# Performance work log

Hardware: AMD Instinct MI355X
Metric: run time of the kernel (lower is better)

The kernel has to match this reference:

```python
import jax, jax.numpy as jnp
import numpy as np

T, B, F_, H, D, C = 16, 1024, 512, 128, 8, 100  # trees, batch, feat, hidden, depth, classes
L = 2 ** (D + 1)  # n_leaf = 512


def _routing_tables():
    # Static per-leaf routing: node index and branch side at each depth.
    # Derived from compute_mu's gather indices:
    #   node(d, l) = 2^d - 1 + l // 2^(D+1-d);  side(d, l) = (l // 2^(D-d)) % 2
    l = np.arange(L)
    node = np.stack([(2 ** d - 1) + l // (2 ** (D + 1 - d)) for d in range(D + 1)])  # [D+1, L]
    side = np.stack([(l // (2 ** (D - d))) % 2 for d in range(D + 1)])               # [D+1, L]
    return jnp.asarray(node, dtype=jnp.int32), jnp.asarray(side.astype(np.bool_))


def setup_inputs() -> dict:
    key = jax.random.key(0)
    ks = jax.random.split(key, 4)
    return {
        "feat": jax.random.normal(ks[0], (B, F_), jnp.float32),
        "W1": jax.random.normal(ks[1], (T, F_, H), jnp.float32) * 0.05,
        "b1": jnp.zeros((T, H), jnp.float32),
        "W2": jax.random.normal(ks[2], (T, H, L), jnp.float32) * 0.05,
        "b2": jnp.zeros((T, L), jnp.float32),
        "pi": jax.random.uniform(ks[3], (T, L, C), jnp.float32, -2.0, 2.0),
    }


def reference(feat, W1, b1, W2, b2, pi):
    node, side = _routing_tables()
    # Per-tree MLP head (dropout is identity in eval mode).
    h = jax.nn.relu(jnp.einsum('bf,tfh->tbh', feat, W1) + b1[:, None, :])        # [T,B,H]
    p = jax.nn.sigmoid(jnp.einsum('tbh,thl->tbl', h, W2) + b2[:, None, :])       # [T,B,L]
    # compute_mu: product of routing probs along each root->leaf path.
    sel = p[:, :, node]                          # [T,B,D+1,L] gather (static indices)
    route = jnp.where(side, 1.0 - sel, sel)      # left -> p, right -> 1-p
    mu = jnp.prod(route, axis=2)                 # [T,B,L]
    # compute_py_x: mean over leaves then mean over trees of mu @ softmax(pi).
    leaf_p = jax.nn.softmax(pi, axis=-1)         # [T,L,C]
    py_x = jnp.einsum('tbl,tlc->bc', mu, leaf_p) / (L * T)  # [B,C]
    return jnp.log(py_x)
```

## Files before the change

### kernel.cpp

```cpp
#include <hip/hip_runtime.h>
#include <hip/hip_bf16.h>
#include <math.h>

#define T_ 16
#define B_ 1024
#define F_ 512
#define H_ 128
#define D_ 8
#define C_ 100
#define L_ 512
#define CP_ 112

typedef __attribute__((ext_vector_type(8))) short bf16x8_t;
typedef __attribute__((ext_vector_type(4))) short bf16x4_t;
typedef __attribute__((ext_vector_type(4))) float f32x4_t;

__device__ inline ushort f2bf(float x) {
  __hip_bfloat16 b = __float2bfloat16(x);
  return *(ushort*)&b;
}
__device__ inline float bf2f(ushort u) {
  union { unsigned int i; float f; } v;
  v.i = ((unsigned int)u) << 16;
  return v.f;
}

__global__ __launch_bounds__(256) void k_prep(
    const float* __restrict__ feat, const float* __restrict__ W1,
    const float* __restrict__ W2, const float* __restrict__ pi,
    ushort* __restrict__ feat_bf, ushort* __restrict__ W1T,
    ushort* __restrict__ W2T, ushort* __restrict__ lp) {
  __shared__ float tile[32][33];
  const int bid = blockIdx.x, tid = threadIdx.x;

  if (bid < 256) {
    int i = (bid * 256 + tid) * 8;
    float4 a = *(const float4*)(feat + i);
    float4 b = *(const float4*)(feat + i + 4);
    bf16x8_t o;
    o[0] = (short)f2bf(a.x); o[1] = (short)f2bf(a.y);
    o[2] = (short)f2bf(a.z); o[3] = (short)f2bf(a.w);
    o[4] = (short)f2bf(b.x); o[5] = (short)f2bf(b.y);
    o[6] = (short)f2bf(b.z); o[7] = (short)f2bf(b.w);
    *(bf16x8_t*)(feat_bf + i) = o;
    return;
  }
  if (bid < 2304) {
    const float* X; ushort* XT; int K, N, kb, nb, s;
    if (bid < 1280) {
      int r = bid - 256;  kb = r & 15; nb = (r >> 4) & 3;  s = r >> 6;
      X = W1; XT = W1T; K = F_; N = H_;
    } else {
      int r = bid - 1280; kb = r & 3;  nb = (r >> 2) & 15; s = r >> 6;
      X = W2; XT = W2T; K = H_; N = L_;
    }
    const int k0 = kb * 32, n0 = nb * 32;
    const int c = tid & 31, r0 = tid >> 5;
    const float* Xs = X + (size_t)s * K * N;
    ushort* XTs = XT + (size_t)s * N * K;
#pragma unroll
    for (int j = 0; j < 4; ++j)
      tile[r0 + 8 * j][c] = Xs[(size_t)(k0 + r0 + 8 * j) * N + n0 + c];
    __syncthreads();
#pragma unroll
    for (int j = 0; j < 4; ++j)
      XTs[(size_t)(n0 + r0 + 8 * j) * K + k0 + c] = f2bf(tile[c][r0 + 8 * j]);
    return;
  }
  {
    int row  = (bid - 2304) * 4 + (tid >> 6);
    int lane = tid & 63;
    const float* x = pi + (size_t)row * C_;
    float v0 = (lane < C_) ? x[lane] : -1e30f;
    float v1 = (lane + 64 < C_) ? x[lane + 64] : -1e30f;
    float m = fmaxf(v0, v1);
#pragma unroll
    for (int off = 32; off; off >>= 1) m = fmaxf(m, __shfl_xor(m, off, 64));
    float e0 = __expf(v0 - m);
    float e1 = (lane + 64 < C_) ? __expf(v1 - m) : 0.0f;
    float sm = e0 + e1;
#pragma unroll
    for (int off = 32; off; off >>= 1) sm += __shfl_xor(sm, off, 64);
    float inv = 1.0f / sm;
    size_t base = (size_t)row * CP_;
    if (lane < C_) lp[base + lane] = f2bf(e0 * inv);
    int c2 = lane + 64;
    if (c2 < CP_) lp[base + c2] = f2bf(c2 < C_ ? e1 * inv : 0.0f);
  }
}

__global__ __launch_bounds__(256) void k12_mfma(
    const ushort* __restrict__ feat, const ushort* __restrict__ W1T,
    const float* __restrict__ b1, const ushort* __restrict__ W2T,
    const float* __restrict__ b2, ushort* __restrict__ mu) {
  __shared__ ushort smem[29696];
  ushort (*h_s)[136] = (ushort(*)[136])smem;
  ushort (*a_s)[72]  = (ushort(*)[72])(smem + 4352);
  ushort (*b_s)[72]  = (ushort(*)[72])(smem + 6656);
  ushort (*w_s)[136] = (ushort(*)[136])(smem + 4352);
  ushort (*p_s)[520] = (ushort(*)[520])(smem + 13056);

  const int t = blockIdx.y, b0 = blockIdx.x * 32, tid = threadIdx.x;
  const int w = tid >> 6, lane = tid & 63, quad = lane >> 4, n = lane & 15;

  {
    f32x4_t acc[2][2];
#pragma unroll
    for (int i = 0; i < 2; ++i)
#pragma unroll
      for (int j = 0; j < 2; ++j) acc[i][j] = (f32x4_t){0.f, 0.f, 0.f, 0.f};

    for (int kc = 0; kc < 8; ++kc) {
      __syncthreads();
      {
        int row = tid >> 3, col8 = (tid & 7) * 8;
        *(bf16x8_t*)&a_s[row][col8] =
            *(const bf16x8_t*)(feat + (size_t)(b0 + row) * F_ + kc * 64 + col8);
      }
#pragma unroll
      for (int i = 0; i < 4; ++i) {
        int idx = i * 256 + tid;
        int row = idx >> 3, col8 = (idx & 7) * 8;
        *(bf16x8_t*)&b_s[row][col8] =
            *(const bf16x8_t*)(W1T + ((size_t)t * H_ + row) * F_ + kc * 64 + col8);
      }
      __syncthreads();
#pragma unroll
      for (int ks = 0; ks < 64; ks += 32) {
        bf16x8_t af[2], bfr[2];
#pragma unroll
        for (int mt = 0; mt < 2; ++mt)
          af[mt] = *(const bf16x8_t*)&a_s[mt * 16 + n][ks + quad * 8];
#pragma unroll
        for (int nt = 0; nt < 2; ++nt)
          bfr[nt] = *(const bf16x8_t*)&b_s[w * 32 + nt * 16 + n][ks + quad * 8];
#pragma unroll
        for (int mt = 0; mt < 2; ++mt)
#pragma unroll
          for (int nt = 0; nt < 2; ++nt)
            acc[mt][nt] = __builtin_amdgcn_mfma_f32_16x16x32_bf16(
                af[mt], bfr[nt], acc[mt][nt], 0, 0, 0);
      }
    }
    float bias[2] = {b1[t * H_ + w * 32 + n], b1[t * H_ + w * 32 + 16 + n]};
#pragma unroll
    for (int mt = 0; mt < 2; ++mt)
#pragma unroll
      for (int nt = 0; nt < 2; ++nt)
#pragma unroll
        for (int r = 0; r < 4; ++r) {
          int row = mt * 16 + quad * 4 + r;
          int col = w * 32 + nt * 16 + n;
          float v = acc[mt][nt][r] + bias[nt];
          h_s[row][col] = f2bf(v > 0.f ? v : 0.f);
        }
  }

  for (int nc = 0; nc < 8; ++nc) {
    __syncthreads();
#pragma unroll
    for (int i = 0; i < 4; ++i) {
      int idx = i * 256 + tid;
      int row = idx >> 4, col8 = (idx & 15) * 8;
      *(bf16x8_t*)&w_s[row][col8] =
          *(const bf16x8_t*)(W2T + ((size_t)t * L_ + nc * 64 + row) * H_ + col8);
    }
    __syncthreads();
    f32x4_t acc[2];
    acc[0] = (f32x4_t){0.f, 0.f, 0.f, 0.f};
    acc[1] = (f32x4_t){0.f, 0.f, 0.f, 0.f};
#pragma unroll
    for (int ks = 0; ks < 128; ks += 32) {
      bf16x8_t bfrag = *(const bf16x8_t*)&w_s[w * 16 + n][ks + quad * 8];
#pragma unroll
      for (int mt = 0; mt < 2; ++mt) {
        bf16x8_t afrag = *(const bf16x8_t*)&h_s[mt * 16 + n][ks + quad * 8];
        acc[mt] = __builtin_amdgcn_mfma_f32_16x16x32_bf16(afrag, bfrag,
                                                          acc[mt], 0, 0, 0);
      }
    }
    int l = nc * 64 + w * 16 + n;
    float bias = b2[t * L_ + l];
#pragma unroll
    for (int mt = 0; mt < 2; ++mt)
#pragma unroll
      for (int r = 0; r < 4; ++r) {
        float x = acc[mt][r] + bias;
        p_s[mt * 16 + quad * 4 + r][l] = f2bf(1.0f / (1.0f + __expf(-x)));
      }
  }
  __syncthreads();

#pragma unroll
  for (int pass = 0; pass < 4; ++pass) {
    int b = pass * 8 + (tid >> 5);
    int s = tid & 31;
    float P = 1.f;
#pragma unroll
    for (int d = 0; d < 5; ++d) {
      int nd = (1 << d) - 1 + (s >> (5 - d));
      int sd = (s >> (4 - d)) & 1;
      float pv = bf2f(p_s[b][nd]);
      P *= sd ? (1.f - pv) : pv;
    }
    float p5 = bf2f(p_s[b][31 + s]);
    float q5[2] = {P * p5, P * (1.f - p5)};
    float q6[4], q7[8];
#pragma unroll
    for (int j = 0; j < 2; ++j) {
      float pv = bf2f(p_s[b][63 + 2 * s + j]);
      q6[2 * j] = q5[j] * pv;
      q6[2 * j + 1] = q5[j] * (1.f - pv);
    }
#pragma unroll
    for (int u = 0; u < 4; ++u) {
      float pv = bf2f(p_s[b][127 + 4 * s + u]);
      q7[2 * u] = q6[u] * pv;
      q7[2 * u + 1] = q6[u] * (1.f - pv);
    }
    bf16x8_t o0, o1;
#pragma unroll
    for (int v = 0; v < 8; ++v) {
      float pv = bf2f(p_s[b][255 + 8 * s + v]);
      ushort e0 = f2bf(q7[v] * pv);
      ushort e1 = f2bf(q7[v] * (1.f - pv));
      if (v < 4) { o0[2 * v] = (short)e0; o0[2 * v + 1] = (short)e1; }
      else       { o1[2 * (v - 4)] = (short)e0; o1[2 * (v - 4) + 1] = (short)e1; }
    }
    ushort* dst = mu + ((size_t)t * B_ + b0 + b) * L_ + s * 16;
    *(bf16x8_t*)dst = o0;
    *(bf16x8_t*)(dst + 8) = o1;
  }
}

__global__ __launch_bounds__(256) void k5_mfma(
    const ushort* __restrict__ mu, const ushort* __restrict__ lp,
    float* __restrict__ part) {
  __shared__ ushort bT[CP_ * 68];
  const int t   = blockIdx.y;
  const int m0  = blockIdx.x * 64;
  const int tid = threadIdx.x;
  const int wave = tid >> 6, lane = tid & 63;
  const int quad = lane >> 4;
  const int n    = lane & 15;
  const int mrow = m0 + wave * 16 + n;

  f32x4_t acc[7];
#pragma unroll
  for (int i = 0; i < 7; ++i) acc[i] = (f32x4_t){0.f, 0.f, 0.f, 0.f};

  const ushort* muRow = mu + ((size_t)t * B_ + mrow) * L_;
  const ushort* lp_t  = lp + (size_t)t * L_ * CP_;

  for (int k0 = 0; k0 < L_; k0 += 64) {
    __syncthreads();
#pragma unroll
    for (int i = 0; i < 28; ++i) {
      int e  = i * 256 + tid;
      int kk = e / CP_;
      int c  = e - kk * CP_;
      bT[c * 68 + kk] = lp_t[(size_t)(k0 + kk) * CP_ + c];
    }
    __syncthreads();
#pragma unroll
    for (int ks = 0; ks < 64; ks += 32) {
      bf16x8_t afrag = *(const bf16x8_t*)(muRow + k0 + ks + quad * 8);
#pragma unroll
      for (int nt = 0; nt < 7; ++nt) {
        const ushort* bb = &bT[(nt * 16 + n) * 68 + ks + quad * 8];
        bf16x4_t lo = *(const bf16x4_t*)(bb);
        bf16x4_t hi = *(const bf16x4_t*)(bb + 4);
        bf16x8_t bfrag;
#pragma unroll
        for (int j = 0; j < 4; ++j) { bfrag[j] = lo[j]; bfrag[4 + j] = hi[j]; }
        acc[nt] = __builtin_amdgcn_mfma_f32_16x16x32_bf16(afrag, bfrag, acc[nt], 0, 0, 0);
      }
    }
  }
#pragma unroll
  for (int nt = 0; nt < 7; ++nt) {
    int c = nt * 16 + n;
    if (c < C_) {
#pragma unroll
      for (int r = 0; r < 4; ++r) {
        int m = m0 + wave * 16 + quad * 4 + r;
        part[((size_t)t * B_ + m) * C_ + c] = acc[nt][r];
      }
    }
  }
}

__global__ __launch_bounds__(256) void k6_log(
    const float* __restrict__ part, float* __restrict__ out) {
  int i = blockIdx.x * 256 + threadIdx.x;
  if (i < B_ * C_) {
    float s = 0.0f;
#pragma unroll
    for (int t = 0; t < T_; ++t) s += part[(size_t)t * B_ * C_ + i];
    out[i] = logf(s * (1.0f / (L_ * T_)));
  }
}

extern "C" void kernel_launch(void* const* d_in, const int* in_sizes, int n_in,
                              void* d_out, int out_size, void* d_ws,
                              size_t ws_size, hipStream_t stream) {
  const float* feat = (const float*)d_in[0];
  const float* W1   = (const float*)d_in[1];
  const float* b1   = (const float*)d_in[2];
  const float* W2   = (const float*)d_in[3];
  const float* b2   = (const float*)d_in[4];
  const float* pi   = (const float*)d_in[5];
  float* out = (float*)d_out;

  char* ws = (char*)d_ws;
  ushort* feat_bf  = (ushort*)(ws);
  ushort* W1T_buf  = (ushort*)(ws + ((size_t)1 << 20));
  ushort* W2T_buf  = (ushort*)(ws + ((size_t)3 << 20));
  ushort* mu_buf   = (ushort*)(ws + ((size_t)5 << 20));
  ushort* leaf_buf = (ushort*)(ws + ((size_t)21 << 20));
  float*  part_buf = (float*)(ws + ((size_t)23 << 20));

  k_prep<<<4352, 256, 0, stream>>>(feat, W1, W2, pi, feat_bf, W1T_buf,
                                   W2T_buf, leaf_buf);
  k12_mfma<<<dim3(B_ / 32, T_), 256, 0, stream>>>(feat_bf, W1T_buf, b1,
                                                  W2T_buf, b2, mu_buf);
  k5_mfma<<<dim3(B_ / 64, T_), 256, 0, stream>>>(mu_buf, leaf_buf, part_buf);
  k6_log<<<(B_ * C_ + 255) / 256, 256, 0, stream>>>(part_buf, out);
}
```

Measured before the change: 114.5 us.

## Fuse mu computation with leaf-distribution GEMM, drop mu round-trip

```diff
diff --git a/kernel.cpp b/kernel.cpp
--- a/kernel.cpp
+++ b/kernel.cpp
@@ -9,10 +9,9 @@
 #define D_ 8
 #define C_ 100
 #define L_ 512
-#define CP_ 112
+#define CPAD 128
 
 typedef __attribute__((ext_vector_type(8))) short bf16x8_t;
-typedef __attribute__((ext_vector_type(4))) short bf16x4_t;
 typedef __attribute__((ext_vector_type(4))) float f32x4_t;
 
 __device__ inline ushort f2bf(float x) {
@@ -29,8 +28,8 @@
     const float* __restrict__ feat, const float* __restrict__ W1,
     const float* __restrict__ W2, const float* __restrict__ pi,
     ushort* __restrict__ feat_bf, ushort* __restrict__ W1T,
-    ushort* __restrict__ W2T, ushort* __restrict__ lp) {
-  __shared__ float tile[32][33];
+    ushort* __restrict__ W2T, ushort* __restrict__ lpT) {
+  __shared__ ushort sm[8320];
   const int bid = blockIdx.x, tid = threadIdx.x;
 
   if (bid < 256) {
@@ -46,6 +45,7 @@
     return;
   }
   if (bid < 2304) {
+    float (*tile)[33] = (float(*)[33])sm;
     const float* X; ushort* XT; int K, N, kb, nb, s;
     if (bid < 1280) {
       int r = bid - 256;  kb = r & 15; nb = (r >> 4) & 3;  s = r >> 6;
@@ -68,37 +68,53 @@
     return;
   }
   {
-    int row  = (bid - 2304) * 4 + (tid >> 6);
-    int lane = tid & 63;
-    const float* x = pi + (size_t)row * C_;
-    float v0 = (lane < C_) ? x[lane] : -1e30f;
-    float v1 = (lane + 64 < C_) ? x[lane + 64] : -1e30f;
-    float m = fmaxf(v0, v1);
-#pragma unroll
-    for (int off = 32; off; off >>= 1) m = fmaxf(m, __shfl_xor(m, off, 64));
-    float e0 = __expf(v0 - m);
-    float e1 = (lane + 64 < C_) ? __expf(v1 - m) : 0.0f;
-    float sm = e0 + e1;
-#pragma unroll
-    for (int off = 32; off; off >>= 1) sm += __shfl_xor(sm, off, 64);
-    float inv = 1.0f / sm;
-    size_t base = (size_t)row * CP_;
-    if (lane < C_) lp[base + lane] = f2bf(e0 * inv);
-    int c2 = lane + 64;
-    if (c2 < CP_) lp[base + c2] = f2bf(c2 < C_ ? e1 * inv : 0.0f);
-  }
-}
-
-__global__ __launch_bounds__(256) void k12_mfma(
+    ushort (*ts)[130] = (ushort(*)[130])sm;
+    const int idx = bid - 2304;
+    const int R0 = idx * 64;
+    const int t = R0 >> 9, li0 = R0 & 511;
+    const int wave = tid >> 6, lane = tid & 63;
+    for (int it = 0; it < 16; ++it) {
+      int r = wave * 16 + it;
+      const float* x = pi + (size_t)(R0 + r) * C_;
+      float v0 = (lane < C_) ? x[lane] : -1e30f;
+      float v1 = (lane + 64 < C_) ? x[lane + 64] : -1e30f;
+      float m = fmaxf(v0, v1);
+#pragma unroll
+      for (int off = 32; off; off >>= 1) m = fmaxf(m, __shfl_xor(m, off, 64));
+      float e0 = __expf(v0 - m);
+      float e1 = (lane + 64 < C_) ? __expf(v1 - m) : 0.0f;
+      float s = e0 + e1;
+#pragma unroll
+      for (int off = 32; off; off >>= 1) s += __shfl_xor(s, off, 64);
+      float inv = 1.0f / s;
+      ts[r][lane]      = (lane < C_) ? f2bf(e0 * inv) : (ushort)0;
+      ts[r][lane + 64] = (lane + 64 < C_) ? f2bf(e1 * inv) : (ushort)0;
+    }
+    __syncthreads();
+    int c = tid >> 1, hf = tid & 1;
+    ushort tmp[32];
+#pragma unroll
+    for (int j = 0; j < 32; ++j) tmp[j] = ts[hf * 32 + j][c];
+    ushort* dst = lpT + ((size_t)t * CPAD + c) * L_ + li0 + hf * 32;
+#pragma unroll
+    for (int j = 0; j < 4; ++j)
+      *(bf16x8_t*)(dst + 8 * j) = *(bf16x8_t*)&tmp[8 * j];
+  }
+}
+
+__global__ __launch_bounds__(256) void k125(
     const ushort* __restrict__ feat, const ushort* __restrict__ W1T,
     const float* __restrict__ b1, const ushort* __restrict__ W2T,
-    const float* __restrict__ b2, ushort* __restrict__ mu) {
-  __shared__ ushort smem[29696];
-  ushort (*h_s)[136] = (ushort(*)[136])smem;
-  ushort (*a_s)[72]  = (ushort(*)[72])(smem + 4352);
-  ushort (*b_s)[72]  = (ushort(*)[72])(smem + 6656);
-  ushort (*w_s)[136] = (ushort(*)[136])(smem + 4352);
-  ushort (*p_s)[520] = (ushort(*)[520])(smem + 13056);
+    const float* __restrict__ b2, const ushort* __restrict__ lpT,
+    float* __restrict__ part) {
+  __shared__ ushort sm[29504];
+  ushort (*a_s)[72]  = (ushort(*)[72]) sm;
+  ushort (*b_s)[72]  = (ushort(*)[72])(sm + 2304);
+  ushort* p_s        = sm;
+  ushort (*h_s)[136] = (ushort(*)[136])(sm + 16448);
+  ushort (*w_s)[136] = (ushort(*)[136])(sm + 20800);
+  ushort (*lp_s)[72] = (ushort(*)[72])(sm + 16448);
+  ushort (*mu_x)[72] = (ushort(*)[72])(sm + 25664);
 
   const int t = blockIdx.y, b0 = blockIdx.x * 32, tid = threadIdx.x;
   const int w = tid >> 6, lane = tid & 63, quad = lane >> 4, n = lane & 15;
@@ -143,6 +159,7 @@
       }
     }
     float bias[2] = {b1[t * H_ + w * 32 + n], b1[t * H_ + w * 32 + 16 + n]};
+    __syncthreads();
 #pragma unroll
     for (int mt = 0; mt < 2; ++mt)
 #pragma unroll
@@ -186,11 +203,12 @@
 #pragma unroll
       for (int r = 0; r < 4; ++r) {
         float x = acc[mt][r] + bias;
-        p_s[mt * 16 + quad * 4 + r][l] = f2bf(1.0f / (1.0f + __expf(-x)));
+        p_s[(mt * 16 + quad * 4 + r) * 514 + l] = f2bf(1.0f / (1.0f + __expf(-x)));
       }
   }
   __syncthreads();
 
+  bf16x8_t muv[4][2];
 #pragma unroll
   for (int pass = 0; pass < 4; ++pass) {
     int b = pass * 8 + (tid >> 5);
@@ -200,94 +218,93 @@
     for (int d = 0; d < 5; ++d) {
       int nd = (1 << d) - 1 + (s >> (5 - d));
       int sd = (s >> (4 - d)) & 1;
-      float pv = bf2f(p_s[b][nd]);
+      float pv = bf2f(p_s[b * 514 + nd]);
       P *= sd ? (1.f - pv) : pv;
     }
-    float p5 = bf2f(p_s[b][31 + s]);
+    float p5 = bf2f(p_s[b * 514 + 31 + s]);
     float q5[2] = {P * p5, P * (1.f - p5)};
     float q6[4], q7[8];
 #pragma unroll
     for (int j = 0; j < 2; ++j) {
-      float pv = bf2f(p_s[b][63 + 2 * s + j]);
+      float pv = bf2f(p_s[b * 514 + 63 + 2 * s + j]);
       q6[2 * j] = q5[j] * pv;
       q6[2 * j + 1] = q5[j] * (1.f - pv);
     }
 #pragma unroll
     for (int u = 0; u < 4; ++u) {
-      float pv = bf2f(p_s[b][127 + 4 * s + u]);
+      float pv = bf2f(p_s[b * 514 + 127 + 4 * s + u]);
       q7[2 * u] = q6[u] * pv;
       q7[2 * u + 1] = q6[u] * (1.f - pv);
     }
     bf16x8_t o0, o1;
 #pragma unroll
     for (int v = 0; v < 8; ++v) {
-      float pv = bf2f(p_s[b][255 + 8 * s + v]);
+      float pv = bf2f(p_s[b * 514 + 255 + 8 * s + v]);
       ushort e0 = f2bf(q7[v] * pv);
       ushort e1 = f2bf(q7[v] * (1.f - pv));
       if (v < 4) { o0[2 * v] = (short)e0; o0[2 * v + 1] = (short)e1; }
       else       { o1[2 * (v - 4)] = (short)e0; o1[2 * (v - 4) + 1] = (short)e1; }
     }
-    ushort* dst = mu + ((size_t)t * B_ + b0 + b) * L_ + s * 16;
-    *(bf16x8_t*)dst = o0;
-    *(bf16x8_t*)(dst + 8) = o1;
-  }
-}
-
-__global__ __launch_bounds__(256) void k5_mfma(
-    const ushort* __restrict__ mu, const ushort* __restrict__ lp,
-    float* __restrict__ part) {
-  __shared__ ushort bT[CP_ * 68];
-  const int t   = blockIdx.y;
-  const int m0  = blockIdx.x * 64;
-  const int tid = threadIdx.x;
-  const int wave = tid >> 6, lane = tid & 63;
-  const int quad = lane >> 4;
-  const int n    = lane & 15;
-  const int mrow = m0 + wave * 16 + n;
-
-  f32x4_t acc[7];
-#pragma unroll
-  for (int i = 0; i < 7; ++i) acc[i] = (f32x4_t){0.f, 0.f, 0.f, 0.f};
-
-  const ushort* muRow = mu + ((size_t)t * B_ + mrow) * L_;
-  const ushort* lp_t  = lp + (size_t)t * L_ * CP_;
-
-  for (int k0 = 0; k0 < L_; k0 += 64) {
-    __syncthreads();
-#pragma unroll
-    for (int i = 0; i < 28; ++i) {
-      int e  = i * 256 + tid;
-      int kk = e / CP_;
-      int c  = e - kk * CP_;
-      bT[c * 68 + kk] = lp_t[(size_t)(k0 + kk) * CP_ + c];
+    muv[pass][0] = o0;
+    muv[pass][1] = o1;
+  }
+
+  f32x4_t acc[2][2];
+#pragma unroll
+  for (int i = 0; i < 2; ++i)
+#pragma unroll
+    for (int j = 0; j < 2; ++j) acc[i][j] = (f32x4_t){0.f, 0.f, 0.f, 0.f};
+
+  const ushort* lpt_t = lpT + (size_t)t * CPAD * L_;
+  for (int c = 0; c < 8; ++c) {
+    {
+      int row = tid >> 1, hf = tid & 1;
+      const ushort* src = lpt_t + (size_t)row * L_ + c * 64 + hf * 32;
+#pragma unroll
+      for (int j = 0; j < 4; ++j)
+        *(bf16x8_t*)&lp_s[row][hf * 32 + 8 * j] = *(const bf16x8_t*)(src + 8 * j);
+    }
+    if (((tid & 31) >> 2) == c) {
+      int sub = tid & 3;
+#pragma unroll
+      for (int pass = 0; pass < 4; ++pass) {
+        int b = pass * 8 + (tid >> 5);
+        *(bf16x8_t*)&mu_x[b][sub * 16]     = muv[pass][0];
+        *(bf16x8_t*)&mu_x[b][sub * 16 + 8] = muv[pass][1];
+      }
     }
     __syncthreads();
 #pragma unroll
     for (int ks = 0; ks < 64; ks += 32) {
-      bf16x8_t afrag = *(const bf16x8_t*)(muRow + k0 + ks + quad * 8);
-#pragma unroll
-      for (int nt = 0; nt < 7; ++nt) {
-        const ushort* bb = &bT[(nt * 16 + n) * 68 + ks + quad * 8];
-        bf16x4_t lo = *(const bf16x4_t*)(bb);
-        bf16x4_t hi = *(const bf16x4_t*)(bb + 4);
-        bf16x8_t bfrag;
-#pragma unroll
-        for (int j = 0; j < 4; ++j) { bfrag[j] = lo[j]; bfrag[4 + j] = hi[j]; }
-        acc[nt] = __builtin_amdgcn_mfma_f32_16x16x32_bf16(afrag, bfrag, acc[nt], 0, 0, 0);
-      }
-    }
-  }
-#pragma unroll
-  for (int nt = 0; nt < 7; ++nt) {
-    int c = nt * 16 + n;
-    if (c < C_) {
-#pragma unroll
-      for (int r = 0; r < 4; ++r) {
-        int m = m0 + wave * 16 + quad * 4 + r;
-        part[((size_t)t * B_ + m) * C_ + c] = acc[nt][r];
-      }
-    }
-  }
+      bf16x8_t af[2], bfr[2];
+#pragma unroll
+      for (int mt = 0; mt < 2; ++mt)
+        af[mt] = *(const bf16x8_t*)&mu_x[mt * 16 + n][ks + quad * 8];
+#pragma unroll
+      for (int nt = 0; nt < 2; ++nt)
+        bfr[nt] = *(const bf16x8_t*)&lp_s[w * 32 + nt * 16 + n][ks + quad * 8];
+#pragma unroll
+      for (int mt = 0; mt < 2; ++mt)
+#pragma unroll
+        for (int nt = 0; nt < 2; ++nt)
+          acc[mt][nt] = __builtin_amdgcn_mfma_f32_16x16x32_bf16(
+              af[mt], bfr[nt], acc[mt][nt], 0, 0, 0);
+    }
+    __syncthreads();
+  }
+#pragma unroll
+  for (int mt = 0; mt < 2; ++mt)
+#pragma unroll
+    for (int nt = 0; nt < 2; ++nt) {
+      int cc = w * 32 + nt * 16 + n;
+      if (cc < C_) {
+#pragma unroll
+        for (int r = 0; r < 4; ++r) {
+          int m = b0 + mt * 16 + quad * 4 + r;
+          part[((size_t)t * B_ + m) * C_ + cc] = acc[mt][nt][r];
+        }
+      }
+    }
 }
 
 __global__ __launch_bounds__(256) void k6_log(
@@ -313,17 +330,15 @@
   float* out = (float*)d_out;
 
   char* ws = (char*)d_ws;
-  ushort* feat_bf  = (ushort*)(ws);
-  ushort* W1T_buf  = (ushort*)(ws + ((size_t)1 << 20));
-  ushort* W2T_buf  = (ushort*)(ws + ((size_t)3 << 20));
-  ushort* mu_buf   = (ushort*)(ws + ((size_t)5 << 20));
-  ushort* leaf_buf = (ushort*)(ws + ((size_t)21 << 20));
-  float*  part_buf = (float*)(ws + ((size_t)23 << 20));
-
-  k_prep<<<4352, 256, 0, stream>>>(feat, W1, W2, pi, feat_bf, W1T_buf,
-                                   W2T_buf, leaf_buf);
-  k12_mfma<<<dim3(B_ / 32, T_), 256, 0, stream>>>(feat_bf, W1T_buf, b1,
-                                                  W2T_buf, b2, mu_buf);
-  k5_mfma<<<dim3(B_ / 64, T_), 256, 0, stream>>>(mu_buf, leaf_buf, part_buf);
+  ushort* feat_bf = (ushort*)(ws);
+  ushort* W1T_buf = (ushort*)(ws + ((size_t)1 << 20));
+  ushort* W2T_buf = (ushort*)(ws + ((size_t)3 << 20));
+  ushort* lpT_buf = (ushort*)(ws + ((size_t)5 << 20));
+  float*  part_buf = (float*)(ws + ((size_t)7 << 20));
+
+  k_prep<<<2432, 256, 0, stream>>>(feat, W1, W2, pi, feat_bf, W1T_buf,
+                                   W2T_buf, lpT_buf);
+  k125<<<dim3(B_ / 32, T_), 256, 0, stream>>>(feat_bf, W1T_buf, b1, W2T_buf,
+                                              b2, lpT_buf, part_buf);
   k6_log<<<(B_ * C_ + 255) / 256, 256, 0, stream>>>(part_buf, out);
 }
```

Result: slower. 116.9 us (+2.0%).
